# Kernel optimization log

Hardware: AMD Instinct MI355X
Metric: run time of the kernel (lower is better)

The kernel has to match this reference:

```python
import jax, jax.numpy as jnp
import numpy as np
from jax import lax

HEADS = 8
DIM_HEAD = 64
INNER = HEADS * DIM_HEAD  # 512
DIM = 256
TOP_K = 512  # top_k=-1 -> Lk // heads = 4096 // 8
LN_EPS = 1e-5


def chan_ln(x, g, b):
    # LayerNorm over channel dim (axis=1) of [b,c,D,H,W]
    mu = jnp.mean(x, axis=1, keepdims=True)
    var = jnp.mean((x - mu) ** 2, axis=1, keepdims=True)
    xn = (x - mu) * lax.rsqrt(var + LN_EPS)
    return xn * g[None, :, None, None, None] + b[None, :, None, None, None]


def l1_cdist(K, Q):
    # K: [B,N,D], Q: [B,M,D] -> [B,N,M]; scan over feature dim to avoid a [B,N,M,D] intermediate
    Kt = jnp.moveaxis(K, -1, 0)  # [D,B,N]
    Qt = jnp.moveaxis(Q, -1, 0)  # [D,B,M]
    acc0 = jnp.zeros((K.shape[0], K.shape[1], Q.shape[1]), K.dtype)
    def step(acc, kq):
        kd, qd = kq
        return acc + jnp.abs(kd[:, :, None] - qd[:, None, :]), None
    acc, _ = lax.scan(step, acc0, (Kt, Qt))
    return acc


def l2norm_ax(t, axis):
    n = jnp.sqrt(jnp.sum(t * t, axis=axis, keepdims=True))
    return t / jnp.maximum(n, 1e-12)


def setup_inputs() -> dict:
    key = jax.random.key(0)
    ks = jax.random.split(key, 12)
    b, Dq, Hq, Wq = 2, 16, 32, 32
    Dc, Hc, Wc = 16, 16, 16
    Lk = Dc * Hc * Wc  # 4096
    return {
        "query_source": jax.random.normal(ks[0], (b, DIM, Dq, Hq, Wq), jnp.float32),
        "context": jax.random.normal(ks[1], (b, DIM, Dc, Hc, Wc), jnp.float32),
        "rand_idx": jax.random.randint(ks[2], (b * HEADS, TOP_K), 0, 4096),
        "g_ctx": jnp.ones((DIM,), jnp.float32),
        "b_ctx": jnp.zeros((DIM,), jnp.float32),
        "g_qs": jnp.ones((DIM,), jnp.float32),
        "b_qs": jnp.zeros((DIM,), jnp.float32),
        "w_kv": jax.random.normal(ks[3], (2 * INNER, DIM), jnp.float32) * 0.02,
        "w_q": jax.random.normal(ks[4], (INNER, DIM), jnp.float32) * 0.02,
        "w_out": jax.random.normal(ks[5], (DIM, INNER), jnp.float32) * 0.02,
        "g_out": jnp.ones((DIM,), jnp.float32),
        "b_out": jnp.zeros((DIM,), jnp.float32),
        "gamma": jnp.full((1,), 0.5, jnp.float32),
    }


def reference(query_source, context, rand_idx, g_ctx, b_ctx, g_qs, b_qs,
              w_kv, w_q, w_out, g_out, b_out, gamma):
    b, c, Dq, Hq, Wq = query_source.shape
    Lq = Dq * Hq * Wq
    Lk = context.shape[2] * context.shape[3] * context.shape[4]

    ctx = chan_ln(context, g_ctx, b_ctx)
    qsn = chan_ln(query_source, g_qs, b_qs)

    # 1x1x1 convs == channel matmuls
    kv = jnp.einsum('oc,bcdhw->bodhw', w_kv, ctx)
    k, v = jnp.split(kv, 2, axis=1)
    q = jnp.einsum('oc,bcdhw->bodhw', w_q, qsn)

    def fold(t):  # [b, inner, ...] -> [b, heads, dim_head, L]
        return t.reshape(t.shape[0], HEADS, DIM_HEAD, -1)
    q, k, v = fold(q), fold(k), fold(v)
    # l2norm over dim_head channels (torch dim=1 after (b h) fold)
    q = l2norm_ax(q, 2)
    k = l2norm_ax(k, 2)
    # -> [b, heads, L, dim_head]
    q = jnp.swapaxes(q, 2, 3)
    k = jnp.swapaxes(k, 2, 3)
    v = jnp.swapaxes(v, 2, 3)

    BH = b * HEADS
    qf = q.reshape(BH, Lq, DIM_HEAD)
    kf = k.reshape(BH, Lk, DIM_HEAD)
    vf = v.reshape(BH, Lk, DIM_HEAD)

    # random-query-anchored token pruning
    Q_small = jnp.take_along_axis(qf, rand_idx[:, :, None], axis=1)  # [BH, TOP_K, dh]
    dist = l1_cdist(kf, Q_small)                                     # [BH, Lk, TOP_K]
    min_d = jnp.min(dist, axis=2)                                    # [BH, Lk]
    _, idx = lax.top_k(-min_d, TOP_K)                                # smallest distances
    ks_sel = jnp.take_along_axis(kf, idx[:, :, None], axis=1)        # [BH, TOP_K, dh]
    vs_sel = jnp.take_along_axis(vf, idx[:, :, None], axis=1)

    ks4 = ks_sel.reshape(b, HEADS, TOP_K, DIM_HEAD)
    vs4 = vs_sel.reshape(b, HEADS, TOP_K, DIM_HEAD)

    # SDPA with scale=1.0, no dropout (eval)
    scores = jnp.einsum('bhqd,bhkd->bhqk', q, ks4)
    attn = jax.nn.softmax(scores, axis=-1)
    out = jnp.einsum('bhqk,bhkd->bhqd', attn, vs4)  # [b,H,Lq,dh]

    out = out.reshape(b, HEADS, Dq, Hq, Wq, DIM_HEAD)
    out = jnp.transpose(out, (0, 1, 5, 2, 3, 4)).reshape(b, INNER, Dq, Hq, Wq)
    out = jnp.einsum('oc,bcdhw->bodhw', w_out, out)
    out = chan_ln(out, g_out, b_out)
    return gamma[0] * out + query_source
```

## Files before the change

kernel.cpp:

```cpp
#include <hip/hip_runtime.h>
#include <hip/hip_bf16.h>
#include <math.h>

#define DIMC  256
#define HEADS 8
#define DH    64
#define INNER 512
#define TOPK  512
#define LQ    16384
#define LKE   4096
#define NB    2
#define NBH   16

typedef __attribute__((ext_vector_type(8))) short bf16x8;
typedef __attribute__((ext_vector_type(4))) float f32x4;
typedef __attribute__((ext_vector_type(16))) unsigned u32x16;

__device__ __forceinline__ unsigned short f2bf(float f) {
    unsigned u = __float_as_uint(f);
    u += 0x7FFFu + ((u >> 16) & 1u);
    return (unsigned short)(u >> 16);
}
__device__ __forceinline__ float bf2f(unsigned short b) {
    return __uint_as_float(((unsigned)b) << 16);
}
__device__ __forceinline__ f32x4 mfma16(bf16x8 a, bf16x8 b, f32x4 c) {
    return __builtin_amdgcn_mfma_f32_16x16x32_bf16(a, b, c, 0, 0, 0);
}
__device__ __forceinline__ unsigned f2q16(float v) {
    return (unsigned)((int)rintf(v * 32000.0f) + 32768) & 0xFFFFu;
}

__global__ void stats_all_kernel(const float* __restrict__ ctx, const float* __restrict__ qs,
                                 float* __restrict__ mu_c, float* __restrict__ rs_c,
                                 float* __restrict__ mu_q, float* __restrict__ rs_q) {
    int idx = blockIdx.x * 256 + threadIdx.x;
    const float* x; float* mu; float* rs; int L; int li;
    if (idx < NB * LKE) { x = ctx; mu = mu_c; rs = rs_c; L = LKE; li = idx; }
    else { li = idx - NB * LKE; if (li >= NB * LQ) return; x = qs; mu = mu_q; rs = rs_q; L = LQ; }
    int b = li / L, l = li - b * L;
    const float* p = x + (size_t)b * DIMC * L + l;
    float s = 0.f, sq = 0.f;
    for (int c = 0; c < DIMC; c++) {
        float v = p[(size_t)c * L];
        s += v; sq += v * v;
    }
    float m = s * (1.0f / DIMC);
    float var = fmaxf(sq * (1.0f / DIMC) - m * m, 0.f);
    mu[li] = m;
    rs[li] = rsqrtf(var + 1e-5f);
}

template<bool WRITELO>
__global__ __launch_bounds__(256) void ln_transpose_kernel(
    const float* __restrict__ x, const float* __restrict__ mu, const float* __restrict__ rs,
    const float* __restrict__ g, const float* __restrict__ beta, int L,
    unsigned short* __restrict__ xhi, unsigned short* __restrict__ xlo) {
    int lt = blockIdx.x, ct = blockIdx.y, b = blockIdx.z;
    int l0 = lt * 64, c0 = ct * 64;
    int t = threadIdx.x;
    __shared__ float T[64][65];
#pragma unroll
    for (int r = 0; r < 16; r++) {
        int f = r * 256 + t;
        int l = f & 63, c = f >> 6;
        int loc = b * L + l0 + l;
        float v = x[((size_t)b * DIMC + c0 + c) * L + l0 + l];
        T[c][l] = (v - mu[loc]) * rs[loc] * g[c0 + c] + beta[c0 + c];
    }
    __syncthreads();
#pragma unroll
    for (int r = 0; r < 16; r++) {
        int f = r * 256 + t;
        int c = f & 63, l = f >> 6;
        float v = T[c][l];
        unsigned short hi = f2bf(v);
        size_t di = ((size_t)b * L + l0 + l) * DIMC + c0 + c;
        xhi[di] = hi;
        if (WRITELO) xlo[di] = f2bf(v - bf2f(hi));
    }
}

template<int MODE>
__global__ __launch_bounds__(256) void gemm_mfma_kernel(
    const float* __restrict__ wmat,
    const unsigned short* __restrict__ xhi, const unsigned short* __restrict__ xlo,
    void* __restrict__ dst0, void* __restrict__ dst1, void* __restrict__ dst2) {
    constexpr int K = 256;
    constexpr int N = (MODE == 0) ? LKE : LQ;
    constexpr bool MAYSPLIT = (MODE == 0);
    int n0 = blockIdx.x * 128;
    int by = blockIdx.y;
    int bb = blockIdx.z;
    int t = threadIdx.x, w = t >> 6, lane = t & 63;
    int wm = w >> 1, wn = w & 1;
    int lanelo = lane & 15, lanehi = lane >> 4;

    __shared__ __align__(16) char Wh[16384];
    __shared__ __align__(16) char Xh[16384];
    __shared__ __align__(16) char Wl[MAYSPLIT ? 16384 : 16];
    __shared__ __align__(16) char Xl[MAYSPLIT ? 16384 : 16];

    bool split = MAYSPLIT && (by < 4);

    const float* wsrc = wmat + (size_t)by * 128 * K;
    const unsigned short* xsh = xhi + ((size_t)bb * N + n0) * K;
    const unsigned short* xsl = xlo + ((size_t)bb * N + n0) * K;

    f32x4 acc[4][4];
#pragma unroll
    for (int mi = 0; mi < 4; mi++)
#pragma unroll
        for (int ni = 0; ni < 4; ni++) acc[mi][ni] = (f32x4){0.f, 0.f, 0.f, 0.f};

    for (int k0 = 0; k0 < K; k0 += 64) {
        if (k0) __syncthreads();
#pragma unroll
        for (int gg = 0; gg < 4; gg++) {
            int e = gg * 2048 + t * 8;
            int row = e >> 6, kc = e & 63;
            const float* wp = wsrc + (size_t)row * K + k0 + kc;
            bf16x8 hi, lo;
#pragma unroll
            for (int i = 0; i < 8; i++) {
                float v = wp[i];
                unsigned short h = f2bf(v);
                hi[i] = (short)h;
                if (MAYSPLIT) lo[i] = (short)f2bf(v - bf2f(h));
            }
            int off = (row * 128 + kc * 2) ^ ((row & 7) << 4);
            *(bf16x8*)(Wh + off) = hi;
            *(bf16x8*)(Xh + off) = *(const bf16x8*)(xsh + (size_t)row * K + k0 + kc);
            if (split) {
                *(bf16x8*)(Wl + off) = lo;
                *(bf16x8*)(Xl + off) = *(const bf16x8*)(xsl + (size_t)row * K + k0 + kc);
            }
        }
        __syncthreads();
#pragma unroll
        for (int kk = 0; kk < 2; kk++) {
            bf16x8 ah[4], bh_[4];
#pragma unroll
            for (int mi = 0; mi < 4; mi++) {
                int row = wm * 64 + mi * 16 + lanelo;
                int off = (row * 128 + kk * 64 + lanehi * 16) ^ ((row & 7) << 4);
                ah[mi] = *(const bf16x8*)(Wh + off);
            }
#pragma unroll
            for (int ni = 0; ni < 4; ni++) {
                int row = wn * 64 + ni * 16 + lanelo;
                int off = (row * 128 + kk * 64 + lanehi * 16) ^ ((row & 7) << 4);
                bh_[ni] = *(const bf16x8*)(Xh + off);
            }
#pragma unroll
            for (int mi = 0; mi < 4; mi++)
#pragma unroll
                for (int ni = 0; ni < 4; ni++)
                    acc[mi][ni] = mfma16(ah[mi], bh_[ni], acc[mi][ni]);
            if (split) {
                bf16x8 al[4], bl_[4];
#pragma unroll
                for (int mi = 0; mi < 4; mi++) {
                    int row = wm * 64 + mi * 16 + lanelo;
                    int off = (row * 128 + kk * 64 + lanehi * 16) ^ ((row & 7) << 4);
                    al[mi] = *(const bf16x8*)(Wl + off);
                }
#pragma unroll
                for (int ni = 0; ni < 4; ni++) {
                    int row = wn * 64 + ni * 16 + lanelo;
                    int off = (row * 128 + kk * 64 + lanehi * 16) ^ ((row & 7) << 4);
                    bl_[ni] = *(const bf16x8*)(Xl + off);
                }
#pragma unroll
                for (int mi = 0; mi < 4; mi++)
#pragma unroll
                    for (int ni = 0; ni < 4; ni++) {
                        acc[mi][ni] = mfma16(ah[mi], bl_[ni], acc[mi][ni]);
                        acc[mi][ni] = mfma16(al[mi], bh_[ni], acc[mi][ni]);
                    }
            }
        }
    }

    bool donorm = (MODE == 1) || (MODE == 0 && by < 4);
    float inv[4];
    if (donorm) {
#pragma unroll
        for (int ni = 0; ni < 4; ni++) {
            float s = 0.f;
#pragma unroll
            for (int mi = 0; mi < 4; mi++)
#pragma unroll
                for (int rg = 0; rg < 4; rg++) s += acc[mi][ni][rg] * acc[mi][ni][rg];
            s += __shfl_xor(s, 16);
            s += __shfl_xor(s, 32);
            inv[ni] = 1.0f / fmaxf(sqrtf(s), 1e-12f);
        }
    }
#pragma unroll
    for (int mi = 0; mi < 4; mi++) {
        int rowg = by * 128 + wm * 64 + mi * 16 + lanehi * 4;
#pragma unroll
        for (int ni = 0; ni < 4; ni++) {
            int l = n0 + wn * 64 + ni * 16 + lanelo;
            if (MODE == 0) {
                bool isk = rowg < 512;
                float sc = isk ? inv[ni] : 1.0f;
                int h = (rowg >> 6) & 7, d0 = rowg & 63;
                float4 v = make_float4(acc[mi][ni][0] * sc, acc[mi][ni][1] * sc,
                                       acc[mi][ni][2] * sc, acc[mi][ni][3] * sc);
                float* dp = isk ? (float*)dst0 : (float*)dst1;
                size_t base = ((size_t)(bb * HEADS + h) * LKE + l) * 64 + d0;
                *(float4*)&dp[base] = v;
                if (isk) {
                    uint2 pk;
                    pk.x = f2q16(v.x) | (f2q16(v.y) << 16);
                    pk.y = f2q16(v.z) | (f2q16(v.w) << 16);
                    *(uint2*)&((unsigned*)dst2)[(((size_t)(bb * HEADS + h) * LKE + l) * 64 + d0) / 2] = pk;
                }
            } else {
                int h = rowg >> 6, d0 = rowg & 63;
                ushort4 u;
                u.x = f2bf(acc[mi][ni][0] * inv[ni]);
                u.y = f2bf(acc[mi][ni][1] * inv[ni]);
                u.z = f2bf(acc[mi][ni][2] * inv[ni]);
                u.w = f2bf(acc[mi][ni][3] * inv[ni]);
                unsigned short* qp = (unsigned short*)dst0;
                *(ushort4*)&qp[((size_t)(bb * HEADS + h) * LQ + l) * 64 + d0] = u;
            }
        }
    }
}

__global__ __launch_bounds__(256) void gemm_out_fused_kernel(
    const float* __restrict__ wmat,
    const unsigned short* __restrict__ afT,
    const float* __restrict__ g, const float* __restrict__ beta,
    const float* __restrict__ gamma, const float* __restrict__ qs_in,
    float* __restrict__ out) {
    int l0 = blockIdx.x * 64;
    int b  = blockIdx.y;
    int t = threadIdx.x, w = t >> 6, lane = t & 63;
    int lanelo = lane & 15, lanehi = lane >> 4;

    __shared__ __align__(16) char Wh[32768];
    __shared__ __align__(16) char Xh[8192];
    __shared__ float sLds[4][64];
    __shared__ float sqLds[4][64];
    __shared__ float gs[256], bs[256];

    gs[t] = g[t];
    bs[t] = beta[t];

    const unsigned short* xs = afT + ((size_t)b * LQ + l0) * 512;

    f32x4 acc[4][4];
#pragma unroll
    for (int mi = 0; mi < 4; mi++)
#pragma unroll
        for (int ni = 0; ni < 4; ni++) acc[mi][ni] = (f32x4){0.f, 0.f, 0.f, 0.f};

    int row0s = t >> 3, c80 = t & 7;
    int row1s = 32 + (t >> 3);
    int offs0 = (row0s * 128 + c80 * 16) ^ ((row0s & 7) << 4);
    int offs1 = (row1s * 128 + c80 * 16) ^ ((row1s & 7) << 4);

    for (int k0 = 0; k0 < 512; k0 += 64) {
        if (k0) __syncthreads();
#pragma unroll
        for (int gg = 0; gg < 8; gg++) {
            int row = gg * 32 + (t >> 3);
            int kc = (t & 7) * 8;
            const float* wp = wmat + (size_t)row * 512 + k0 + kc;
            bf16x8 hi;
#pragma unroll
            for (int i = 0; i < 8; i++) hi[i] = (short)f2bf(wp[i]);
            int off = (row * 128 + kc * 2) ^ ((row & 7) << 4);
            *(bf16x8*)(Wh + off) = hi;
        }
        *(bf16x8*)(Xh + offs0) = *(const bf16x8*)(xs + (size_t)row0s * 512 + k0 + c80 * 8);
        *(bf16x8*)(Xh + offs1) = *(const bf16x8*)(xs + (size_t)row1s * 512 + k0 + c80 * 8);
        __syncthreads();
#pragma unroll
        for (int kk = 0; kk < 2; kk++) {
            bf16x8 ah[4], bh_[4];
#pragma unroll
            for (int mi = 0; mi < 4; mi++) {
                int row = w * 64 + mi * 16 + lanelo;
                int off = (row * 128 + kk * 64 + lanehi * 16) ^ ((row & 7) << 4);
                ah[mi] = *(const bf16x8*)(Wh + off);
            }
#pragma unroll
            for (int ni = 0; ni < 4; ni++) {
                int row = ni * 16 + lanelo;
                int off = (row * 128 + kk * 64 + lanehi * 16) ^ ((row & 7) << 4);
                bh_[ni] = *(const bf16x8*)(Xh + off);
            }
#pragma unroll
            for (int mi = 0; mi < 4; mi++)
#pragma unroll
                for (int ni = 0; ni < 4; ni++)
                    acc[mi][ni] = mfma16(ah[mi], bh_[ni], acc[mi][ni]);
        }
    }

#pragma unroll
    for (int ni = 0; ni < 4; ni++) {
        float s = 0.f, sq = 0.f;
#pragma unroll
        for (int mi = 0; mi < 4; mi++)
#pragma unroll
            for (int rg = 0; rg < 4; rg++) {
                float v = acc[mi][ni][rg];
                s += v; sq += v * v;
            }
        s += __shfl_xor(s, 16);  s += __shfl_xor(s, 32);
        sq += __shfl_xor(sq, 16); sq += __shfl_xor(sq, 32);
        if (lanehi == 0) {
            sLds[w][ni * 16 + lanelo] = s;
            sqLds[w][ni * 16 + lanelo] = sq;
        }
    }
    __syncthreads();
    float mu_[4], rs_[4];
#pragma unroll
    for (int ni = 0; ni < 4; ni++) {
        int l = ni * 16 + lanelo;
        float s  = (sLds[0][l] + sLds[1][l]) + (sLds[2][l] + sLds[3][l]);
        float sq = (sqLds[0][l] + sqLds[1][l]) + (sqLds[2][l] + sqLds[3][l]);
        float m = s * (1.0f / 256.0f);
        float var = fmaxf(sq * (1.0f / 256.0f) - m * m, 0.f);
        mu_[ni] = m;
        rs_[ni] = rsqrtf(var + 1e-5f);
    }
    float gm = gamma[0];
#pragma unroll
    for (int mi = 0; mi < 4; mi++) {
#pragma unroll
        for (int ni = 0; ni < 4; ni++) {
            int l = ni * 16 + lanelo;
#pragma unroll
            for (int rg = 0; rg < 4; rg++) {
                int ch = w * 64 + mi * 16 + lanehi * 4 + rg;
                float xn = (acc[mi][ni][rg] - mu_[ni]) * rs_[ni] * gs[ch] + bs[ch];
                size_t oi = ((size_t)(b * DIMC + ch)) * LQ + l0 + l;
                out[oi] = gm * xn + qs_in[oi];
            }
        }
    }
}

__global__ __launch_bounds__(256) void qsample_kernel(
    const float* __restrict__ x, const float* __restrict__ mu, const float* __restrict__ rs,
    const float* __restrict__ g, const float* __restrict__ beta,
    const float* __restrict__ w, const int* __restrict__ ridx,
    unsigned* __restrict__ Qint) {
    int lt = blockIdx.x, bh = blockIdx.y;
    int b = bh >> 3, h = bh & 7;
    int t = threadIdx.x, tx = t & 15, ty = t >> 4;
    __shared__ float Ws[64][33];
    __shared__ float Xs[32][65];
    __shared__ float Cs[64][65];
    __shared__ float nf[64];
    __shared__ int lidx[64];
    if (t < 64) lidx[t] = ridx[bh * TOPK + lt * 64 + t];
    __syncthreads();
    float acc[4][4];
#pragma unroll
    for (int a = 0; a < 4; a++)
#pragma unroll
        for (int c2 = 0; c2 < 4; c2++) acc[a][c2] = 0.f;
    for (int kc = 0; kc < DIMC; kc += 32) {
#pragma unroll
        for (int r = 0; r < 8; r++) {
            int f = r * 256 + t;
            int oi = f >> 5, kj = f & 31;
            Ws[oi][kj] = w[(size_t)(h * 64 + oi) * DIMC + kc + kj];
        }
#pragma unroll
        for (int r = 0; r < 8; r++) {
            int f = r * 256 + t;
            int kj = f >> 6, lj = f & 63;
            int l = lidx[lj];
            int loc = b * LQ + l;
            float v = x[(size_t)b * DIMC * LQ + (size_t)(kc + kj) * LQ + l];
            Xs[kj][lj] = (v - mu[loc]) * rs[loc] * g[kc + kj] + beta[kc + kj];
        }
        __syncthreads();
#pragma unroll
        for (int kj = 0; kj < 32; kj++) {
            float wr[4], xr[4];
#pragma unroll
            for (int a = 0; a < 4; a++) wr[a] = Ws[ty * 4 + a][kj];
#pragma unroll
            for (int c2 = 0; c2 < 4; c2++) xr[c2] = Xs[kj][tx * 4 + c2];
#pragma unroll
            for (int a = 0; a < 4; a++)
#pragma unroll
                for (int c2 = 0; c2 < 4; c2++) acc[a][c2] += wr[a] * xr[c2];
        }
        __syncthreads();
    }
#pragma unroll
    for (int a = 0; a < 4; a++)
#pragma unroll
        for (int c2 = 0; c2 < 4; c2++) Cs[ty * 4 + a][tx * 4 + c2] = acc[a][c2];
    __syncthreads();
    if (t < 64) {
        float sq = 0.f;
        for (int o = 0; o < 64; o++) { float v = Cs[o][t]; sq += v * v; }
        nf[t] = 1.0f / fmaxf(sqrtf(sq), 1e-12f);
    }
    __syncthreads();
#pragma unroll
    for (int r = 0; r < 8; r++) {
        int f = r * 256 + t;
        int dp = f & 31, lj = f >> 5;
        float v0 = Cs[dp * 2][lj] * nf[lj];
        float v1 = Cs[dp * 2 + 1][lj] * nf[lj];
        Qint[((size_t)bh * TOPK + (size_t)lt * 64 + lj) * 32 + dp] =
            f2q16(v0) | (f2q16(v1) << 16);
    }
}

__global__ __launch_bounds__(256) __attribute__((amdgpu_waves_per_eu(4, 4)))
void cdist_sad_kernel(
    const unsigned* __restrict__ kint,
    const unsigned* __restrict__ Qint,
    unsigned* __restrict__ min_d4) {
    int bh = blockIdx.y;
    int key = blockIdx.x * 256 + threadIdx.x;
    int qz = blockIdx.z;
    const unsigned* kp = kint + ((size_t)bh * LKE + key) * 32;
    unsigned k[32];
#pragma unroll
    for (int d8 = 0; d8 < 8; d8++) {
        uint4 v = *(const uint4*)(kp + d8 * 4);
        k[d8 * 4 + 0] = v.x; k[d8 * 4 + 1] = v.y;
        k[d8 * 4 + 2] = v.z; k[d8 * 4 + 3] = v.w;
    }
#pragma unroll
    for (int d = 0; d < 32; d++) asm volatile("" : "+v"(k[d]));

    unsigned long long qaddr = (unsigned long long)(const void*)
        (Qint + ((size_t)bh * TOPK + (size_t)qz * (TOPK / 4)) * 32);
    u32x16 qa0, qa1, qb0, qb1;
    asm volatile(
        "s_load_dwordx16 %0, %2, 0x00\n\t"
        "s_load_dwordx16 %1, %2, 0x40"
        : "=s"(qa0), "=s"(qa1) : "s"(qaddr));
    unsigned best = 0xFFFFFFFFu;

#define S1(ACC, KK, QQ) asm("v_sad_u16 %0, %1, %2, %0" : "+v"(ACC) : "v"(KK), "s"(QQ));
#define S16(QV, KB) \
    S1(a0, k[KB + 0], QV[0])  S1(a1, k[KB + 1], QV[1]) \
    S1(a2, k[KB + 2], QV[2])  S1(a3, k[KB + 3], QV[3]) \
    S1(a0, k[KB + 4], QV[4])  S1(a1, k[KB + 5], QV[5]) \
    S1(a2, k[KB + 6], QV[6])  S1(a3, k[KB + 7], QV[7]) \
    S1(a0, k[KB + 8], QV[8])  S1(a1, k[KB + 9], QV[9]) \
    S1(a2, k[KB + 10], QV[10]) S1(a3, k[KB + 11], QV[11]) \
    S1(a0, k[KB + 12], QV[12]) S1(a1, k[KB + 13], QV[13]) \
    S1(a2, k[KB + 14], QV[14]) S1(a3, k[KB + 15], QV[15])

    for (int qi = 0; qi < TOPK / 4; qi += 2) {
        asm volatile(
            "s_load_dwordx16 %0, %2, 0x80\n\t"
            "s_load_dwordx16 %1, %2, 0xc0"
            : "=s"(qb0), "=s"(qb1) : "s"(qaddr));
        asm volatile("s_waitcnt lgkmcnt(2)" : "+s"(qa0), "+s"(qa1));
        {
            unsigned a0 = 0, a1 = 0, a2 = 0, a3 = 0;
            S16(qa0, 0) S16(qa1, 16)
            best = min(best, (a0 + a1) + (a2 + a3));
        }
        qaddr += 256;
        asm volatile(
            "s_load_dwordx16 %0, %2, 0x00\n\t"
            "s_load_dwordx16 %1, %2, 0x40"
            : "=s"(qa0), "=s"(qa1) : "s"(qaddr));
        asm volatile("s_waitcnt lgkmcnt(2)" : "+s"(qb0), "+s"(qb1));
        {
            unsigned a0 = 0, a1 = 0, a2 = 0, a3 = 0;
            S16(qb0, 0) S16(qb1, 16)
            best = min(best, (a0 + a1) + (a2 + a3));
        }
    }
#undef S16
#undef S1
    min_d4[((size_t)qz * NBH + bh) * LKE + key] = best;
}

__global__ void select_topk_kernel(const unsigned* __restrict__ min_d4, int* __restrict__ isel) {
    int bh = blockIdx.x;
    int t = threadIdx.x;
    __shared__ unsigned su[LKE];
    __shared__ int hist[256];
    __shared__ int scan[256];
    __shared__ int sb[2];
    for (int i = t; i < LKE; i += 256) {
        unsigned a = min(min_d4[(size_t)bh * LKE + i],
                         min_d4[(size_t)(NBH + bh) * LKE + i]);
        unsigned b = min(min_d4[(size_t)(2 * NBH + bh) * LKE + i],
                         min_d4[(size_t)(3 * NBH + bh) * LKE + i]);
        su[i] = min(a, b);
    }
    unsigned prefix = 0, mask = 0;
    int need = TOPK;
    for (int shift = 24; shift >= 0; shift -= 8) {
        hist[t] = 0;
        __syncthreads();
        for (int i = t; i < LKE; i += 256) {
            unsigned u = su[i];
            if ((u & mask) == prefix) atomicAdd(&hist[(u >> shift) & 255], 1);
        }
        __syncthreads();
        scan[t] = hist[t];
        __syncthreads();
#pragma unroll
        for (int d = 1; d < 256; d <<= 1) {
            int v = (t >= d) ? scan[t - d] : 0;
            __syncthreads();
            scan[t] += v;
            __syncthreads();
        }
        int excl = (t == 0) ? 0 : scan[t - 1];
        if (scan[t] >= need && excl < need) {
            sb[0] = t;
            sb[1] = need - excl;
        }
        __syncthreads();
        prefix |= ((unsigned)sb[0]) << shift;
        mask |= (255u << shift);
        need = sb[1];
        __syncthreads();
    }
    if (t < 64) {
        int pos = 0, eqseen = 0;
        unsigned long long lanem1 = (t == 0) ? 0ull : ((1ull << t) - 1ull);
        for (int i0 = 0; i0 < LKE; i0 += 64) {
            unsigned u = su[i0 + t];
            bool lt = (u < prefix);
            bool eq = (u == prefix);
            unsigned long long be = __ballot(eq);
            int eqbefore = __popcll(be & lanem1);
            bool take = lt || (eq && (eqseen + eqbefore) < need);
            unsigned long long bt = __ballot(take);
            if (take) isel[bh * TOPK + pos + __popcll(bt & lanem1)] = i0 + t;
            pos += __popcll(bt);
            eqseen += __popcll(be);
        }
    }
}

__global__ __launch_bounds__(256) void gather_kv_kernel(
    const float* __restrict__ kf, const float* __restrict__ vf,
    const int* __restrict__ isel,
    unsigned short* __restrict__ kselh, unsigned short* __restrict__ vTh) {
    int bh = blockIdx.y, kc = blockIdx.x * 64;
    int t = threadIdx.x;
    __shared__ float T[64][65];
    __shared__ int rows[64];
    if (t < 64) rows[t] = isel[bh * TOPK + kc + t];
    __syncthreads();
#pragma unroll
    for (int r = 0; r < 16; r++) {
        int f = r * 256 + t;
        int key = f >> 6, d = f & 63;
        kselh[((size_t)bh * TOPK + kc + key) * 64 + d] =
            f2bf(kf[((size_t)bh * LKE + rows[key]) * 64 + d]);
    }
#pragma unroll
    for (int r = 0; r < 4; r++) {
        int c = r * 256 + t;
        int row = c >> 4, c4 = c & 15;
        float4 v = *(const float4*)(vf + ((size_t)bh * LKE + rows[row]) * 64 + c4 * 4);
        T[row][c4 * 4 + 0] = v.x; T[row][c4 * 4 + 1] = v.y;
        T[row][c4 * 4 + 2] = v.z; T[row][c4 * 4 + 3] = v.w;
    }
    __syncthreads();
#pragma unroll
    for (int r = 0; r < 16; r++) {
        int f = r * 256 + t;
        int d = f >> 6, key = f & 63;
        vTh[(size_t)bh * 64 * TOPK + (size_t)d * TOPK + kc + key] = f2bf(T[key][d]);
    }
}

__global__ __launch_bounds__(256) void attn_mfma_kernel(
    const unsigned short* __restrict__ qh,
    const unsigned short* __restrict__ kselh,
    const unsigned short* __restrict__ vTh,
    unsigned short* __restrict__ afT) {
    int bh = blockIdx.y, rt = blockIdx.x;
    int bq = bh >> 3, h = bh & 7;
    int t = threadIdx.x, w = t >> 6, lane = t & 63;
    __shared__ unsigned short Ks[2][64 * 64];
    __shared__ unsigned short Vts[2][64 * 64];
    __shared__ unsigned short Ps[4][2][16 * 64];

    const unsigned short* qb = qh + ((size_t)bh * LQ + (size_t)rt * 128) * 64;
    const unsigned short* kb = kselh + (size_t)bh * TOPK * 64;
    const unsigned short* vb = vTh + (size_t)bh * 64 * TOPK;

    int lanelo = lane & 15, lanehi = lane >> 4;

    int row0s = t >> 3, c80 = t & 7;
    int row1s = 32 + (t >> 3), c81 = t & 7;
    int offs0 = (row0s * 128 + c80 * 16) ^ ((row0s & 7) << 4);
    int offs1 = (row1s * 128 + c81 * 16) ^ ((row1s & 7) << 4);

    bf16x8 qfrag[2][2];
#pragma unroll
    for (int s = 0; s < 2; s++)
#pragma unroll
        for (int kk = 0; kk < 2; kk++) {
            int row = s * 64 + w * 16 + lanelo;
            qfrag[s][kk] = *(const bf16x8*)(qb + (size_t)row * 64 + kk * 32 + lanehi * 8);
        }

    {
        *(bf16x8*)((char*)Ks[0] + offs0) = *(const bf16x8*)(kb + row0s * 64 + c80 * 8);
        *(bf16x8*)((char*)Ks[0] + offs1) = *(const bf16x8*)(kb + row1s * 64 + c81 * 8);
        *(bf16x8*)((char*)Vts[0] + offs0) = *(const bf16x8*)(vb + row0s * TOPK + c80 * 8);
        *(bf16x8*)((char*)Vts[0] + offs1) = *(const bf16x8*)(vb + row1s * TOPK + c81 * 8);
    }
    __syncthreads();

    f32x4 o[2][4];
#pragma unroll
    for (int s = 0; s < 2; s++)
#pragma unroll
        for (int m = 0; m < 4; m++) o[s][m] = (f32x4){0.f, 0.f, 0.f, 0.f};
    float part[2][4] = {{0.f, 0.f, 0.f, 0.f}, {0.f, 0.f, 0.f, 0.f}};
    int cur = 0;

    for (int ch = 0; ch < 8; ch++) {
        bf16x8 knx0, knx1, vnx0, vnx1;
        if (ch < 7) {
            int kc0 = (ch + 1) * 64;
            knx0 = *(const bf16x8*)(kb + (kc0 + row0s) * 64 + c80 * 8);
            knx1 = *(const bf16x8*)(kb + (kc0 + row1s) * 64 + c81 * 8);
            vnx0 = *(const bf16x8*)(vb + row0s * TOPK + kc0 + c80 * 8);
            vnx1 = *(const bf16x8*)(vb + row1s * TOPK + kc0 + c81 * 8);
        }
        bf16x8 kfr[4][2];
#pragma unroll
        for (int n = 0; n < 4; n++)
#pragma unroll
            for (int kk = 0; kk < 2; kk++) {
                int row = n * 16 + lanelo;
                kfr[n][kk] = *(const bf16x8*)((char*)Ks[cur] +
                    ((row * 128 + kk * 64 + lanehi * 16) ^ ((row & 7) << 4)));
            }
#pragma unroll
        for (int s = 0; s < 2; s++) {
            f32x4 sv[4];
#pragma unroll
            for (int n = 0; n < 4; n++) {
                sv[n] = (f32x4){0.f, 0.f, 0.f, 0.f};
#pragma unroll
                for (int kk = 0; kk < 2; kk++)
                    sv[n] = mfma16(qfrag[s][kk], kfr[n][kk], sv[n]);
            }
            unsigned short* pw = Ps[w][s];
#pragma unroll
            for (int n = 0; n < 4; n++) {
#pragma unroll
                for (int rg = 0; rg < 4; rg++) {
                    float p = __expf(sv[n][rg]);
                    unsigned short ph = (unsigned short)(__float_as_uint(p) >> 16);
                    part[s][rg] += bf2f(ph);
                    int row = lanehi * 4 + rg, col = n * 16 + lanelo;
                    *(unsigned short*)((char*)pw +
                        ((row * 128 + col * 2) ^ ((row & 7) << 4))) = ph;
                }
            }
        }
        bf16x8 vfr[4][2];
#pragma unroll
        for (int m = 0; m < 4; m++)
#pragma unroll
            for (int kk = 0; kk < 2; kk++) {
                int row = m * 16 + lanelo;
                vfr[m][kk] = *(const bf16x8*)((char*)Vts[cur] +
                    ((row * 128 + kk * 64 + lanehi * 16) ^ ((row & 7) << 4)));
            }
#pragma unroll
        for (int s = 0; s < 2; s++) {
            bf16x8 pfrag[2];
#pragma unroll
            for (int kk = 0; kk < 2; kk++) {
                int row = lanelo;
                pfrag[kk] = *(const bf16x8*)((char*)Ps[w][s] +
                    ((row * 128 + kk * 64 + lanehi * 16) ^ ((row & 7) << 4)));
            }
#pragma unroll
            for (int m = 0; m < 4; m++)
#pragma unroll
                for (int kk = 0; kk < 2; kk++)
                    o[s][m] = mfma16(pfrag[kk], vfr[m][kk], o[s][m]);
        }
        if (ch < 7) {
            *(bf16x8*)((char*)Ks[cur ^ 1] + offs0) = knx0;
            *(bf16x8*)((char*)Ks[cur ^ 1] + offs1) = knx1;
            *(bf16x8*)((char*)Vts[cur ^ 1] + offs0) = vnx0;
            *(bf16x8*)((char*)Vts[cur ^ 1] + offs1) = vnx1;
        }
        __syncthreads();
        cur ^= 1;
    }
#pragma unroll
    for (int s = 0; s < 2; s++) {
#pragma unroll
        for (int rg = 0; rg < 4; rg++) {
            float v = part[s][rg];
            v += __shfl_xor(v, 1); v += __shfl_xor(v, 2);
            v += __shfl_xor(v, 4); v += __shfl_xor(v, 8);
            float invs = 1.0f / v;
            int l = rt * 128 + s * 64 + w * 16 + lanehi * 4 + rg;
            size_t base = ((size_t)bq * LQ + l) * 512 + h * 64 + lanelo;
#pragma unroll
            for (int m = 0; m < 4; m++)
                afT[base + m * 16] = f2bf(o[s][m][rg] * invs);
        }
    }
}

extern "C" void kernel_launch(void* const* d_in, const int* in_sizes, int n_in,
                              void* d_out, int out_size, void* d_ws, size_t ws_size,
                              hipStream_t stream) {
    const float* qs_in = (const float*)d_in[0];
    const float* ctx   = (const float*)d_in[1];
    const int*   ridx  = (const int*)d_in[2];
    const float* g_ctx = (const float*)d_in[3];
    const float* b_ctx = (const float*)d_in[4];
    const float* g_qs  = (const float*)d_in[5];
    const float* b_qs  = (const float*)d_in[6];
    const float* w_kv  = (const float*)d_in[7];
    const float* w_q   = (const float*)d_in[8];
    const float* w_out = (const float*)d_in[9];
    const float* g_out = (const float*)d_in[10];
    const float* b_out = (const float*)d_in[11];
    const float* gamma = (const float*)d_in[12];
    float* out = (float*)d_out;

    char* ws = (char*)d_ws;
    size_t off = 0;
    auto alloc = [&](size_t bytes) { char* p = ws + off; off += (bytes + 255) & ~(size_t)255; return p; };

    float*          kf    = (float*)alloc((size_t)NBH * LKE * 64 * 4);
    float*          vf    = (float*)alloc((size_t)NBH * LKE * 64 * 4);
    unsigned*       kint  = (unsigned*)alloc((size_t)NBH * LKE * 32 * 4);
    unsigned short* qh    = (unsigned short*)alloc((size_t)NBH * LQ * 64 * 2);
    char*           uni   = alloc((size_t)NB * LQ * INNER * 2);
    unsigned short* ctxT_hi = (unsigned short*)(uni);
    unsigned short* ctxT_lo = (unsigned short*)(uni + (size_t)NB * LKE * DIMC * 2);
    unsigned short* qsT_hi  = (unsigned short*)(uni + (size_t)2 * NB * LKE * DIMC * 2);
    unsigned short* afT     = (unsigned short*)(uni);

    unsigned*       Qint  = (unsigned*)alloc((size_t)NBH * TOPK * 32 * 4);
    unsigned short* kselh = (unsigned short*)alloc((size_t)NBH * TOPK * 64 * 2);
    unsigned short* vTh   = (unsigned short*)alloc((size_t)NBH * 64 * TOPK * 2);
    unsigned*       min_d4= (unsigned*)alloc((size_t)4 * NBH * LKE * 4);
    float*          mu_c  = (float*)alloc(NB * LKE * 4);
    float*          rs_c  = (float*)alloc(NB * LKE * 4);
    float*          mu_q  = (float*)alloc(NB * LQ * 4);
    float*          rs_q  = (float*)alloc(NB * LQ * 4);
    int*            isel  = (int*)alloc(NBH * TOPK * 4);

    stats_all_kernel<<<(NB * (LKE + LQ)) / 256, 256, 0, stream>>>(
        ctx, qs_in, mu_c, rs_c, mu_q, rs_q);
    ln_transpose_kernel<true><<<dim3(LKE / 64, DIMC / 64, NB), 256, 0, stream>>>(
        ctx, mu_c, rs_c, g_ctx, b_ctx, LKE, ctxT_hi, ctxT_lo);
    ln_transpose_kernel<false><<<dim3(LQ / 64, DIMC / 64, NB), 256, 0, stream>>>(
        qs_in, mu_q, rs_q, g_qs, b_qs, LQ, qsT_hi, nullptr);
    gemm_mfma_kernel<0><<<dim3(LKE / 128, 8, NB), 256, 0, stream>>>(
        w_kv, ctxT_hi, ctxT_lo, kf, vf, kint);
    gemm_mfma_kernel<1><<<dim3(LQ / 128, 4, NB), 256, 0, stream>>>(
        w_q, qsT_hi, qsT_hi, qh, nullptr, nullptr);
    qsample_kernel<<<dim3(TOPK / 64, NBH), 256, 0, stream>>>(
        qs_in, mu_q, rs_q, g_qs, b_qs, w_q, ridx, Qint);
    cdist_sad_kernel<<<dim3(LKE / 256, NBH, 4), 256, 0, stream>>>(kint, Qint, min_d4);
    select_topk_kernel<<<NBH, 256, 0, stream>>>(min_d4, isel);
    gather_kv_kernel<<<dim3(TOPK / 64, NBH), 256, 0, stream>>>(kf, vf, isel, kselh, vTh);
    attn_mfma_kernel<<<dim3(LQ / 128, NBH), 256, 0, stream>>>(qh, kselh, vTh, afT);
    gemm_out_fused_kernel<<<dim3(LQ / 64, NB), 256, 0, stream>>>(
        w_out, afT, g_out, b_out, gamma, qs_in, out);
}
```

Before: 299.0 us.

## Load K/V MFMA fragments directly from global memory, dropping LDS staging

The attention kernel no longer stages K and V chunks through double-buffered shared memory with block-wide barriers. Each wave now reads its MFMA operand fragments straight from global memory, relying on L1/L2 caching, since all waves share the same small K/V per head. This removes the LDS stores, the per-chunk __syncthreads and part of the LDS footprint. The cost is four times the global/L1 load traffic (every wave reloads the same data) and exposed load latency, because the loads are no longer prefetched one chunk ahead.

```diff
diff --git a/kernel.cpp b/kernel.cpp
--- a/kernel.cpp
+++ b/kernel.cpp
@@ -594,8 +594,6 @@
     int bh = blockIdx.y, rt = blockIdx.x;
     int bq = bh >> 3, h = bh & 7;
     int t = threadIdx.x, w = t >> 6, lane = t & 63;
-    __shared__ unsigned short Ks[2][64 * 64];
-    __shared__ unsigned short Vts[2][64 * 64];
     __shared__ unsigned short Ps[4][2][16 * 64];
 
     const unsigned short* qb = qh + ((size_t)bh * LQ + (size_t)rt * 128) * 64;
@@ -604,11 +602,6 @@
 
     int lanelo = lane & 15, lanehi = lane >> 4;
 
-    int row0s = t >> 3, c80 = t & 7;
-    int row1s = 32 + (t >> 3), c81 = t & 7;
-    int offs0 = (row0s * 128 + c80 * 16) ^ ((row0s & 7) << 4);
-    int offs1 = (row1s * 128 + c81 * 16) ^ ((row1s & 7) << 4);
-
     bf16x8 qfrag[2][2];
 #pragma unroll
     for (int s = 0; s < 2; s++)
@@ -618,40 +611,21 @@
             qfrag[s][kk] = *(const bf16x8*)(qb + (size_t)row * 64 + kk * 32 + lanehi * 8);
         }
 
-    {
-        *(bf16x8*)((char*)Ks[0] + offs0) = *(const bf16x8*)(kb + row0s * 64 + c80 * 8);
-        *(bf16x8*)((char*)Ks[0] + offs1) = *(const bf16x8*)(kb + row1s * 64 + c81 * 8);
-        *(bf16x8*)((char*)Vts[0] + offs0) = *(const bf16x8*)(vb + row0s * TOPK + c80 * 8);
-        *(bf16x8*)((char*)Vts[0] + offs1) = *(const bf16x8*)(vb + row1s * TOPK + c81 * 8);
-    }
-    __syncthreads();
-
     f32x4 o[2][4];
 #pragma unroll
     for (int s = 0; s < 2; s++)
 #pragma unroll
         for (int m = 0; m < 4; m++) o[s][m] = (f32x4){0.f, 0.f, 0.f, 0.f};
     float part[2][4] = {{0.f, 0.f, 0.f, 0.f}, {0.f, 0.f, 0.f, 0.f}};
-    int cur = 0;
 
     for (int ch = 0; ch < 8; ch++) {
-        bf16x8 knx0, knx1, vnx0, vnx1;
-        if (ch < 7) {
-            int kc0 = (ch + 1) * 64;
-            knx0 = *(const bf16x8*)(kb + (kc0 + row0s) * 64 + c80 * 8);
-            knx1 = *(const bf16x8*)(kb + (kc0 + row1s) * 64 + c81 * 8);
-            vnx0 = *(const bf16x8*)(vb + row0s * TOPK + kc0 + c80 * 8);
-            vnx1 = *(const bf16x8*)(vb + row1s * TOPK + kc0 + c81 * 8);
-        }
         bf16x8 kfr[4][2];
 #pragma unroll
         for (int n = 0; n < 4; n++)
 #pragma unroll
-            for (int kk = 0; kk < 2; kk++) {
-                int row = n * 16 + lanelo;
-                kfr[n][kk] = *(const bf16x8*)((char*)Ks[cur] +
-                    ((row * 128 + kk * 64 + lanehi * 16) ^ ((row & 7) << 4)));
-            }
+            for (int kk = 0; kk < 2; kk++)
+                kfr[n][kk] = *(const bf16x8*)(
+                    kb + (size_t)(ch * 64 + n * 16 + lanelo) * 64 + kk * 32 + lanehi * 8);
 #pragma unroll
         for (int s = 0; s < 2; s++) {
             f32x4 sv[4];
@@ -680,11 +654,9 @@
 #pragma unroll
         for (int m = 0; m < 4; m++)
 #pragma unroll
-            for (int kk = 0; kk < 2; kk++) {
-                int row = m * 16 + lanelo;
-                vfr[m][kk] = *(const bf16x8*)((char*)Vts[cur] +
-                    ((row * 128 + kk * 64 + lanehi * 16) ^ ((row & 7) << 4)));
-            }
+            for (int kk = 0; kk < 2; kk++)
+                vfr[m][kk] = *(const bf16x8*)(
+                    vb + (size_t)(m * 16 + lanelo) * TOPK + ch * 64 + kk * 32 + lanehi * 8);
 #pragma unroll
         for (int s = 0; s < 2; s++) {
             bf16x8 pfrag[2];
@@ -700,14 +672,6 @@
                 for (int kk = 0; kk < 2; kk++)
                     o[s][m] = mfma16(pfrag[kk], vfr[m][kk], o[s][m]);
         }
-        if (ch < 7) {
-            *(bf16x8*)((char*)Ks[cur ^ 1] + offs0) = knx0;
-            *(bf16x8*)((char*)Ks[cur ^ 1] + offs1) = knx1;
-            *(bf16x8*)((char*)Vts[cur ^ 1] + offs0) = vnx0;
-            *(bf16x8*)((char*)Vts[cur ^ 1] + offs1) = vnx1;
-        }
-        __syncthreads();
-        cur ^= 1;
     }
 #pragma unroll
     for (int s = 0; s < 2; s++) {
```

Measured after the change: 359.1 us. +20.1%, slower.
